# Kernel tuning notes

Measured on AMD Instinct MI355X. Metric: run time of the kernel, lower is better.

The kernel has to match this reference:

```python
import jax, jax.numpy as jnp
import numpy as np

WPB = [4, 2, 2]          # words_per_block per scale
NH = 8                   # num_heads
DIM = 256                # feature dim (uniform, required by cross-scale einsums)
HD = DIM // NH           # per-head feature dim
W_PAR, W_PEER, W_KID = 0.5, 1.0, 2.0


def _linear(x, W):
    # torch nn.Linear (no bias): W is [out, in]
    return jnp.einsum('bhwi,oi->bhwo', x, W)


def _split_heads(y):
    # 'b h w (k f) -> b k h w f'
    b, H, Wd, D = y.shape
    return jnp.transpose(y.reshape(b, H, Wd, NH, D // NH), (0, 3, 1, 2, 4))


def _query(x, W):
    return _split_heads(_linear(x, W))


def _kv(x, W):
    # 'b h w (i k f) -> i b k h w f' with i=2
    y = _linear(x, W)
    b, H, Wd, D = y.shape
    y = y.reshape(b, H, Wd, 2, NH, D // (2 * NH))
    y = jnp.transpose(y, (3, 0, 4, 1, 2, 5))
    return y[0], y[1]


def _blocks(x, hb):
    # 'b k (h1 h2) (w1 w2) f -> b k h1 w1 (h2 w2) f'
    b, k, H, Wd, f = x.shape
    h1, w1 = H // hb, Wd // hb
    x = x.reshape(b, k, h1, hb, w1, hb, f)
    return jnp.transpose(x, (0, 1, 2, 4, 3, 5, 6)).reshape(b, k, h1, w1, hb * hb, f)


def _forward(xs, qpeer, kvpeer, qpar, kvpar, qkid, kvkid):
    n = len(WPB)
    outs = []
    for i in range(n):
        hb = WPB[i]
        hk = WPB[i + 1] if i < n - 1 else 0
        npar = 1 if i > 0 else 0
        scale = (hb + npar + hk) ** -0.5  # coupled scaling (decouple_scales=False)
        x = xs[i]
        b, Hi, Wi, _ = x.shape
        h1, w1 = Hi // hb, Wi // hb
        L = hb * hb  # queries per block
        attn, val, wts = [], [], []
        # --- peers ---
        qp = _blocks(_query(x, qpeer[i]), hb)
        kp, vp = _kv(x, kvpeer[i])
        kp, vp = _blocks(kp, hb), _blocks(vp, hb)
        attn.append(jnp.einsum('bkhwlf,bkhwmf->bkhwlm', qp, kp) * scale)
        val.append(jnp.broadcast_to(vp[:, :, :, :, None], (b, NH, h1, w1, L, L, HD)))
        wts.append(W_PEER * jnp.ones((L,), jnp.float32))
        # --- parents ---
        if i > 0:
            qpa = _blocks(_query(x, qpar[i - 1]), hb)
            kpa, vpa = _kv(xs[i - 1], kvpar[i - 1])  # [b,k,h1,w1,f]
            attn.append(jnp.einsum('bkhwlf,bkhwf->bkhwl', qpa, kpa)[..., None] * scale)
            val.append(jnp.broadcast_to(vpa[:, :, :, :, None, None, :], (b, NH, h1, w1, L, 1, HD)))
            wts.append(W_PAR * jnp.ones((1,), jnp.float32))
        # --- kids ---
        if i < n - 1:
            g = hk * hk
            qk = _query(x, qkid[i])               # [b,k,Hi,Wi,f]
            kk, vk = _kv(xs[i + 1], kvkid[i])
            kkb = _blocks(kk, hk)                  # [b,k,Hi,Wi,g,f]
            a = jnp.einsum('bkhwf,bkhwgf->bkhwg', qk, kkb) * scale
            a = jnp.transpose(a.reshape(b, NH, h1, hb, w1, hb, g), (0, 1, 2, 4, 3, 5, 6)).reshape(b, NH, h1, w1, L, g)
            attn.append(a)
            vkb = vk.reshape(b, NH, h1, hb, hk, w1, hb, hk, HD)
            vkb = jnp.transpose(vkb, (0, 1, 2, 5, 3, 6, 4, 7, 8)).reshape(b, NH, h1, w1, L, g, HD)
            val.append(vkb)
            wts.append(W_KID * jnp.ones((g,), jnp.float32))
        V = jnp.concatenate(val, axis=-2)          # [b,k,h1,w1,L,M,f]
        wvec = jnp.concatenate(wts)                # [M]
        A = jax.nn.softmax(jnp.concatenate(attn, axis=-1), axis=-1)
        A = wvec * A
        A = A / A.sum(-1, keepdims=True)
        # NOTE: faithful to the source einsum 'bkhwlm,bkhwlnf->bkhwlf' where m and n
        # are independently summed indices (attn row-sum times value sum over n).
        o = jnp.einsum('bkhwlm,bkhwlnf->bkhwlf', A, V)
        # 'b k h1 w1 (h2 w2) f -> b (h1 h2) (w1 w2) (k f)'
        o = jnp.transpose(o.reshape(b, NH, h1, w1, hb, hb, HD), (0, 2, 4, 3, 5, 1, 6)).reshape(b, Hi, Wi, NH * HD)
        outs.append(o)
    # forward returns ms_proj_drop(ms_slf_attn): projection output is discarded in the
    # source (ms_out is overwritten), and dropout is identity at p=0.
    return tuple(outs)


def setup_inputs() -> dict:
    key = jax.random.key(0)
    ks = iter(jax.random.split(key, 24))
    B = 8
    Hs = [16, 32, 64]
    d = {}
    for i in range(3):
        d[f'x{i}'] = jax.random.normal(next(ks), (B, Hs[i], Hs[i], DIM), jnp.float32)
    for i in range(3):
        d[f'qpeer_w{i}'] = 0.02 * jax.random.normal(next(ks), (DIM, DIM), jnp.float32)
        d[f'kvpeer_w{i}'] = 0.02 * jax.random.normal(next(ks), (2 * DIM, DIM), jnp.float32)
    for i in (1, 2):
        d[f'qpar_w{i}'] = 0.02 * jax.random.normal(next(ks), (DIM, DIM), jnp.float32)
        d[f'kvpar_w{i}'] = 0.02 * jax.random.normal(next(ks), (2 * DIM, DIM), jnp.float32)
    for i in (0, 1):
        d[f'qkid_w{i}'] = 0.02 * jax.random.normal(next(ks), (DIM, DIM), jnp.float32)
        d[f'kvkid_w{i}'] = 0.02 * jax.random.normal(next(ks), (2 * DIM, DIM), jnp.float32)
    return d


def reference(x0, x1, x2, qpeer_w0, qpeer_w1, qpeer_w2, kvpeer_w0, kvpeer_w1, kvpeer_w2,
              qpar_w1, qpar_w2, kvpar_w1, kvpar_w2, qkid_w0, qkid_w1, kvkid_w0, kvkid_w1):
    return _forward([x0, x1, x2],
                    [qpeer_w0, qpeer_w1, qpeer_w2],
                    [kvpeer_w0, kvpeer_w1, kvpeer_w2],
                    [qpar_w1, qpar_w2],
                    [kvpar_w1, kvpar_w2],
                    [qkid_w0, qkid_w1],
                    [kvkid_w0, kvkid_w1])
```

## Files before the change

### kernel.cpp

```cpp
#include <hip/hip_runtime.h>


constexpr int FD = 256;

typedef __attribute__((ext_vector_type(8))) short short8;
typedef __attribute__((ext_vector_type(4))) float floatx4;

__device__ inline unsigned short bf16bits(float f) {
  unsigned u = __builtin_bit_cast(unsigned, f);
  return (unsigned short)((u + 0x7fffu + ((u >> 16) & 1u)) >> 16);
}
__device__ inline ushort4 cvt4(float4 v) {
  ushort4 o;
  o.x = bf16bits(v.x); o.y = bf16bits(v.y);
  o.z = bf16bits(v.z); o.w = bf16bits(v.w);
  return o;
}

constexpr size_t OFF_S1 = 144 * 256;
constexpr size_t OFF_S2 = OFF_S1 + 2048 * 256;
constexpr size_t OFF_W = OFF_S2 + 8192 * 256;
constexpr size_t OFF_X0 = OFF_W + 7 * 65536;
constexpr size_t OFF_X1 = OFF_X0 + 2048 * 256;

__global__ __launch_bounds__(256) void prep(
    const float4* __restrict__ x0, const float4* __restrict__ x1,
    const float4* __restrict__ x2, const float* __restrict__ wp0,
    const float* __restrict__ wk0, const float* __restrict__ wp1,
    const float* __restrict__ wq1, const float* __restrict__ wk1,
    const float* __restrict__ wp2, const float* __restrict__ wq2,
    unsigned short* __restrict__ ws) {
  int blk = blockIdx.x;
  int t = threadIdx.x;
  if (blk < 2592) {
    const float4* x;
    unsigned short* S;
    unsigned short* xo = nullptr;
    int Hs, Ws, hb, row0;
    if (blk < 32) {
      x = x0; S = ws; xo = ws + OFF_X0; Hs = 4; Ws = 4; hb = 4; row0 = blk * 4;
    } else if (blk < 544) {
      x = x1; S = ws + OFF_S1; xo = ws + OFF_X1;
      Hs = 16; Ws = 16; hb = 2; row0 = (blk - 32) * 4;
    } else {
      x = x2; S = ws + OFF_S2; Hs = 32; Ws = 32; hb = 2; row0 = (blk - 544) * 4;
    }
    int c = t & 63;
    int row = row0 + (t >> 6);
    int bw = row % Ws;
    int t2 = row / Ws;
    int bh = t2 % Hs;
    int b = t2 / Hs;
    int W = Ws * hb;
    size_t base4 = (((size_t)b * Hs * hb + bh * hb) * W + bw * hb) * 64 + c;
    const float4* xb = x + base4;
    float4 s = {0.f, 0.f, 0.f, 0.f};
    for (int i = 0; i < hb; ++i)
      for (int j = 0; j < hb; ++j) {
        float4 v = xb[(size_t)(i * W + j) * 64];
        s.x += v.x; s.y += v.y; s.z += v.z; s.w += v.w;
        if (xo) *(ushort4*)(xo + (base4 + (size_t)(i * W + j) * 64) * 4) = cvt4(v);
      }
    *(ushort4*)(S + (size_t)row * FD + c * 4) = cvt4(s);
  } else {
    int wb = blk - 2592;
    int mat = wb >> 6;
    int row = (wb & 63) * 4 + (t >> 6);
    int c4 = (t & 63) * 4;
    const float* src;
    switch (mat) {
      case 0: src = wp0; break;
      case 1: src = wk0; break;
      case 2: src = wp1; break;
      case 3: src = wq1; break;
      case 4: src = wk1; break;
      case 5: src = wp2; break;
      default: src = wq2; break;
    }
    float4 v = *(const float4*)(src + (size_t)(256 + row) * FD + c4);
    *(ushort4*)(ws + OFF_W + (size_t)mat * 65536 + (size_t)row * FD + c4) =
        cvt4(v);
  }
}

#define MFMA(a, b, c) __builtin_amdgcn_mfma_f32_16x16x32_bf16(a, b, c, 0, 0, 0)

__global__ __launch_bounds__(256) void gemm(const unsigned short* __restrict__ ws,
                                            float* __restrict__ out0,
                                            float* __restrict__ out1,
                                            float* __restrict__ out2) {
  __shared__ float lds[4][16][17];
  int t = threadIdx.x;
  int l = t & 63;
  int wv = t >> 6;
  int c = l & 15, q = l >> 4;
  const short8* Wb = (const short8*)(ws + OFF_W);

  if (blockIdx.x < 512) {
    int r0 = (blockIdx.x >> 2) * 64;
    int n0 = (blockIdx.x & 3) * 64;
    int n = n0 + wv * 16 + c;
    const short8* S2b = (const short8*)(ws + OFF_S2);
    const short8* X1b = (const short8*)(ws + OFF_X1);
    int cb0 = (r0 >> 10) * 256 + (((r0 >> 5) & 31) >> 1) * 16;
    const short8* aS1 = (const short8*)(ws + OFF_S1) + (size_t)(cb0 + c) * 32 + q;
    const short8* aX0 = (const short8*)(ws + OFF_X0) + (size_t)(cb0 + c) * 32 + q;
    const short8 *aS2[4], *aX1[4];
#pragma unroll
    for (int mt = 0; mt < 4; ++mt) {
      aS2[mt] = S2b + (size_t)(r0 + mt * 16 + c) * 32 + q;
      aX1[mt] = X1b + (size_t)(r0 + mt * 16 + c) * 32 + q;
    }
    const short8* bK1 = Wb + (size_t)4 * 8192 + (size_t)n * 32 + q;
    const short8* bP2 = Wb + (size_t)5 * 8192 + (size_t)n * 32 + q;
    const short8* bQ2 = Wb + (size_t)6 * 8192 + (size_t)n * 32 + q;
    const short8* bP1 = Wb + (size_t)2 * 8192 + (size_t)n * 32 + q;
    const short8* bQ1 = Wb + (size_t)3 * 8192 + (size_t)n * 32 + q;
    floatx4 accK[4] = {0, 0, 0, 0};
    floatx4 accC2[4] = {0, 0, 0, 0};
    floatx4 accC1 = {0, 0, 0, 0};
#pragma unroll 2
    for (int kk = 0; kk < 8; ++kk) {
      short8 k1 = bK1[kk * 4], p2 = bP2[kk * 4], q2 = bQ2[kk * 4];
      short8 p1 = bP1[kk * 4], q1 = bQ1[kk * 4];
      accC1 = MFMA(aS1[kk * 4], p1, accC1);
      accC1 = MFMA(aX0[kk * 4], q1, accC1);
#pragma unroll
      for (int mt = 0; mt < 4; ++mt) {
        short8 a = aS2[mt][kk * 4];
        accK[mt] = MFMA(a, k1, accK[mt]);
        accC2[mt] = MFMA(a, p2, accC2[mt]);
        accC2[mt] = MFMA(aX1[mt][kk * 4], q2, accC2[mt]);
      }
    }
#pragma unroll
    for (int r = 0; r < 4; ++r) lds[wv][4 * q + r][c] = accC1[r];
    __syncthreads();
#pragma unroll
    for (int mt = 0; mt < 4; ++mt)
#pragma unroll
      for (int r = 0; r < 4; ++r) {
        int rg = r0 + mt * 16 + 4 * q + r;
        int w = rg & 31;
        out1[(size_t)rg * FD + n] = accK[mt][r] + lds[wv][w >> 1][c];
        int b = rg >> 10, h = (rg >> 5) & 31;
        size_t o = ((size_t)b * 4096 + h * 128 + 2 * w) * FD + n;
        float v = accC2[mt][r];
        out2[o] = v;
        out2[o + FD] = v;
        out2[o + 16384] = v;
        out2[o + 16384 + FD] = v;
      }
  } else {
    int bid = blockIdx.x - 512;
    int r0 = (bid >> 2) * 64;
    int n0 = (bid & 3) * 64;
    int n = n0 + wv * 16 + c;
    const short8* S1b = (const short8*)(ws + OFF_S1);
    const short8* aC = (const short8*)ws + (size_t)((r0 >> 4) + c) * 32 + q;
    const short8* bK = Wb + (size_t)1 * 8192 + (size_t)n * 32 + q;
    const short8* bP = Wb + (size_t)0 * 8192 + (size_t)n * 32 + q;
    const short8* aS[4];
#pragma unroll
    for (int mt = 0; mt < 4; ++mt)
      aS[mt] = S1b + (size_t)(r0 + mt * 16 + c) * 32 + q;
    floatx4 accK[4] = {0, 0, 0, 0};
    floatx4 accC = {0, 0, 0, 0};
#pragma unroll 2
    for (int kk = 0; kk < 8; ++kk) {
      short8 b0 = bK[kk * 4], b1 = bP[kk * 4];
      accC = MFMA(aC[kk * 4], b1, accC);
#pragma unroll
      for (int mt = 0; mt < 4; ++mt) accK[mt] = MFMA(aS[mt][kk * 4], b0, accK[mt]);
    }
    float s0 = __shfl(accC[0], c), s1 = __shfl(accC[1], c);
    float s2 = __shfl(accC[2], c), s3 = __shfl(accC[3], c);
    float cv = q == 0 ? s0 : q == 1 ? s1 : q == 2 ? s2 : s3;
#pragma unroll
    for (int mt = 0; mt < 4; ++mt)
#pragma unroll
      for (int r = 0; r < 4; ++r)
        out0[(size_t)(r0 + mt * 16 + 4 * q + r) * FD + n] = accK[mt][r] + cv;
  }
}

extern "C" void kernel_launch(void* const* d_in, const int* in_sizes, int n_in,
                              void* d_out, int out_size, void* d_ws,
                              size_t ws_size, hipStream_t stream) {
  const float* x0 = (const float*)d_in[0];
  const float* x1 = (const float*)d_in[1];
  const float* x2 = (const float*)d_in[2];

  const float *kvpeer0, *kvpeer1, *kvpeer2, *kvpar1, *kvpar2, *kvkid0, *kvkid1;
  if (n_in > 4 && in_sizes[4] == 2 * FD * FD) {
    kvpeer0 = (const float*)d_in[4];
    kvpeer1 = (const float*)d_in[6];
    kvpeer2 = (const float*)d_in[8];
    kvpar1 = (const float*)d_in[10];
    kvpar2 = (const float*)d_in[12];
    kvkid0 = (const float*)d_in[14];
    kvkid1 = (const float*)d_in[16];
  } else {
    kvpeer0 = (const float*)d_in[6];
    kvpeer1 = (const float*)d_in[7];
    kvpeer2 = (const float*)d_in[8];
    kvpar1 = (const float*)d_in[11];
    kvpar2 = (const float*)d_in[12];
    kvkid0 = (const float*)d_in[15];
    kvkid1 = (const float*)d_in[16];
  }

  unsigned short* ws = (unsigned short*)d_ws;
  float* out0 = (float*)d_out;
  float* out1 = out0 + (size_t)8 * 16 * 16 * FD;
  float* out2 = out1 + (size_t)8 * 32 * 32 * FD;

  prep<<<3040, 256, 0, stream>>>((const float4*)x0, (const float4*)x1,
                                 (const float4*)x2, kvpeer0, kvkid0, kvpeer1,
                                 kvpar1, kvkid1, kvpeer2, kvpar2, ws);
  gemm<<<640, 256, 0, stream>>>(ws, out0, out1, out2);
}
```

Before: 167.7 us.

## Split scale-2 GEMM into separate out1/out2 blocks with register-preloaded operands

```diff
diff --git a/kernel.cpp b/kernel.cpp
--- a/kernel.cpp
+++ b/kernel.cpp
@@ -85,10 +85,9 @@
 
 #define MFMA(a, b, c) __builtin_amdgcn_mfma_f32_16x16x32_bf16(a, b, c, 0, 0, 0)
 
-__global__ __launch_bounds__(256) void gemm(const unsigned short* __restrict__ ws,
-                                            float* __restrict__ out0,
-                                            float* __restrict__ out1,
-                                            float* __restrict__ out2) {
+__global__ __launch_bounds__(256, 2) void gemm(
+    const unsigned short* __restrict__ ws, float* __restrict__ out0,
+    float* __restrict__ out1, float* __restrict__ out2) {
   __shared__ float lds[4][16][17];
   int t = threadIdx.x;
   int l = t & 63;
@@ -100,87 +99,136 @@
     int r0 = (blockIdx.x >> 2) * 64;
     int n0 = (blockIdx.x & 3) * 64;
     int n = n0 + wv * 16 + c;
+    const short8* bP = Wb + (size_t)5 * 8192 + (size_t)n * 32 + q;
+    const short8* bQ = Wb + (size_t)6 * 8192 + (size_t)n * 32 + q;
+    short8 Bp[8], Bq[8];
+#pragma unroll
+    for (int kk = 0; kk < 8; ++kk) {
+      Bp[kk] = bP[kk * 4];
+      Bq[kk] = bQ[kk * 4];
+    }
     const short8* S2b = (const short8*)(ws + OFF_S2);
     const short8* X1b = (const short8*)(ws + OFF_X1);
-    int cb0 = (r0 >> 10) * 256 + (((r0 >> 5) & 31) >> 1) * 16;
-    const short8* aS1 = (const short8*)(ws + OFF_S1) + (size_t)(cb0 + c) * 32 + q;
-    const short8* aX0 = (const short8*)(ws + OFF_X0) + (size_t)(cb0 + c) * 32 + q;
-    const short8 *aS2[4], *aX1[4];
 #pragma unroll
     for (int mt = 0; mt < 4; ++mt) {
-      aS2[mt] = S2b + (size_t)(r0 + mt * 16 + c) * 32 + q;
-      aX1[mt] = X1b + (size_t)(r0 + mt * 16 + c) * 32 + q;
-    }
-    const short8* bK1 = Wb + (size_t)4 * 8192 + (size_t)n * 32 + q;
-    const short8* bP2 = Wb + (size_t)5 * 8192 + (size_t)n * 32 + q;
-    const short8* bQ2 = Wb + (size_t)6 * 8192 + (size_t)n * 32 + q;
-    const short8* bP1 = Wb + (size_t)2 * 8192 + (size_t)n * 32 + q;
-    const short8* bQ1 = Wb + (size_t)3 * 8192 + (size_t)n * 32 + q;
-    floatx4 accK[4] = {0, 0, 0, 0};
-    floatx4 accC2[4] = {0, 0, 0, 0};
-    floatx4 accC1 = {0, 0, 0, 0};
-#pragma unroll 2
-    for (int kk = 0; kk < 8; ++kk) {
-      short8 k1 = bK1[kk * 4], p2 = bP2[kk * 4], q2 = bQ2[kk * 4];
-      short8 p1 = bP1[kk * 4], q1 = bQ1[kk * 4];
-      accC1 = MFMA(aS1[kk * 4], p1, accC1);
-      accC1 = MFMA(aX0[kk * 4], q1, accC1);
-#pragma unroll
-      for (int mt = 0; mt < 4; ++mt) {
-        short8 a = aS2[mt][kk * 4];
-        accK[mt] = MFMA(a, k1, accK[mt]);
-        accC2[mt] = MFMA(a, p2, accC2[mt]);
-        accC2[mt] = MFMA(aX1[mt][kk * 4], q2, accC2[mt]);
-      }
-    }
-#pragma unroll
-    for (int r = 0; r < 4; ++r) lds[wv][4 * q + r][c] = accC1[r];
-    __syncthreads();
-#pragma unroll
-    for (int mt = 0; mt < 4; ++mt)
+      const short8* aS = S2b + (size_t)(r0 + mt * 16 + c) * 32 + q;
+      const short8* aX = X1b + (size_t)(r0 + mt * 16 + c) * 32 + q;
+      short8 As[8], Ax[8];
+#pragma unroll
+      for (int kk = 0; kk < 8; ++kk) {
+        As[kk] = aS[kk * 4];
+        Ax[kk] = aX[kk * 4];
+      }
+      floatx4 acc = {0, 0, 0, 0};
+#pragma unroll
+      for (int kk = 0; kk < 8; ++kk) {
+        acc = MFMA(As[kk], Bp[kk], acc);
+        acc = MFMA(Ax[kk], Bq[kk], acc);
+      }
 #pragma unroll
       for (int r = 0; r < 4; ++r) {
         int rg = r0 + mt * 16 + 4 * q + r;
-        int w = rg & 31;
-        out1[(size_t)rg * FD + n] = accK[mt][r] + lds[wv][w >> 1][c];
-        int b = rg >> 10, h = (rg >> 5) & 31;
+        int b = rg >> 10, h = (rg >> 5) & 31, w = rg & 31;
         size_t o = ((size_t)b * 4096 + h * 128 + 2 * w) * FD + n;
-        float v = accC2[mt][r];
+        float v = acc[r];
         out2[o] = v;
         out2[o + FD] = v;
         out2[o + 16384] = v;
         out2[o + 16384 + FD] = v;
       }
-  } else {
+    }
+  } else if (blockIdx.x < 1024) {
     int bid = blockIdx.x - 512;
     int r0 = (bid >> 2) * 64;
     int n0 = (bid & 3) * 64;
     int n = n0 + wv * 16 + c;
-    const short8* S1b = (const short8*)(ws + OFF_S1);
-    const short8* aC = (const short8*)ws + (size_t)((r0 >> 4) + c) * 32 + q;
+    const short8* bK = Wb + (size_t)4 * 8192 + (size_t)n * 32 + q;
+    const short8* bP = Wb + (size_t)2 * 8192 + (size_t)n * 32 + q;
+    const short8* bQ = Wb + (size_t)3 * 8192 + (size_t)n * 32 + q;
+    short8 Bk[8], Bp[8], Bq[8];
+#pragma unroll
+    for (int kk = 0; kk < 8; ++kk) {
+      Bk[kk] = bK[kk * 4];
+      Bp[kk] = bP[kk * 4];
+      Bq[kk] = bQ[kk * 4];
+    }
+    int cb0 = (r0 >> 10) * 256 + (((r0 >> 5) & 31) >> 1) * 16;
+    {
+      const short8* aS1 =
+          (const short8*)(ws + OFF_S1) + (size_t)(cb0 + c) * 32 + q;
+      const short8* aX0 =
+          (const short8*)(ws + OFF_X0) + (size_t)(cb0 + c) * 32 + q;
+      short8 A1[8], A0[8];
+#pragma unroll
+      for (int kk = 0; kk < 8; ++kk) {
+        A1[kk] = aS1[kk * 4];
+        A0[kk] = aX0[kk * 4];
+      }
+      floatx4 accC = {0, 0, 0, 0};
+#pragma unroll
+      for (int kk = 0; kk < 8; ++kk) {
+        accC = MFMA(A1[kk], Bp[kk], accC);
+        accC = MFMA(A0[kk], Bq[kk], accC);
+      }
+#pragma unroll
+      for (int r = 0; r < 4; ++r) lds[wv][4 * q + r][c] = accC[r];
+    }
+    const short8* S2b = (const short8*)(ws + OFF_S2);
+#pragma unroll
+    for (int mt = 0; mt < 4; ++mt) {
+      const short8* aS = S2b + (size_t)(r0 + mt * 16 + c) * 32 + q;
+      short8 As[8];
+#pragma unroll
+      for (int kk = 0; kk < 8; ++kk) As[kk] = aS[kk * 4];
+      floatx4 acc = {0, 0, 0, 0};
+#pragma unroll
+      for (int kk = 0; kk < 8; ++kk) acc = MFMA(As[kk], Bk[kk], acc);
+#pragma unroll
+      for (int r = 0; r < 4; ++r) {
+        int rg = r0 + mt * 16 + 4 * q + r;
+        int w = rg & 31;
+        out1[(size_t)rg * FD + n] = acc[r] + lds[wv][w >> 1][c];
+      }
+    }
+  } else {
+    int bid = blockIdx.x - 1024;
+    int r0 = (bid >> 2) * 64;
+    int n0 = (bid & 3) * 64;
+    int n = n0 + wv * 16 + c;
     const short8* bK = Wb + (size_t)1 * 8192 + (size_t)n * 32 + q;
     const short8* bP = Wb + (size_t)0 * 8192 + (size_t)n * 32 + q;
-    const short8* aS[4];
-#pragma unroll
-    for (int mt = 0; mt < 4; ++mt)
-      aS[mt] = S1b + (size_t)(r0 + mt * 16 + c) * 32 + q;
-    floatx4 accK[4] = {0, 0, 0, 0};
+    short8 Bk[8], Bp[8];
+#pragma unroll
+    for (int kk = 0; kk < 8; ++kk) {
+      Bk[kk] = bK[kk * 4];
+      Bp[kk] = bP[kk * 4];
+    }
     floatx4 accC = {0, 0, 0, 0};
-#pragma unroll 2
-    for (int kk = 0; kk < 8; ++kk) {
-      short8 b0 = bK[kk * 4], b1 = bP[kk * 4];
-      accC = MFMA(aC[kk * 4], b1, accC);
-#pragma unroll
-      for (int mt = 0; mt < 4; ++mt) accK[mt] = MFMA(aS[mt][kk * 4], b0, accK[mt]);
+    {
+      const short8* aC = (const short8*)ws + (size_t)((r0 >> 4) + c) * 32 + q;
+      short8 AC[8];
+#pragma unroll
+      for (int kk = 0; kk < 8; ++kk) AC[kk] = aC[kk * 4];
+#pragma unroll
+      for (int kk = 0; kk < 8; ++kk) accC = MFMA(AC[kk], Bp[kk], accC);
     }
     float s0 = __shfl(accC[0], c), s1 = __shfl(accC[1], c);
     float s2 = __shfl(accC[2], c), s3 = __shfl(accC[3], c);
     float cv = q == 0 ? s0 : q == 1 ? s1 : q == 2 ? s2 : s3;
-#pragma unroll
-    for (int mt = 0; mt < 4; ++mt)
+    const short8* S1b = (const short8*)(ws + OFF_S1);
+#pragma unroll
+    for (int mt = 0; mt < 4; ++mt) {
+      const short8* aS = S1b + (size_t)(r0 + mt * 16 + c) * 32 + q;
+      short8 As[8];
+#pragma unroll
+      for (int kk = 0; kk < 8; ++kk) As[kk] = aS[kk * 4];
+      floatx4 acc = {0, 0, 0, 0};
+#pragma unroll
+      for (int kk = 0; kk < 8; ++kk) acc = MFMA(As[kk], Bk[kk], acc);
 #pragma unroll
       for (int r = 0; r < 4; ++r)
-        out0[(size_t)(r0 + mt * 16 + 4 * q + r) * FD + n] = accK[mt][r] + cv;
+        out0[(size_t)(r0 + mt * 16 + 4 * q + r) * FD + n] = acc[r] + cv;
+    }
   }
 }
 
@@ -218,5 +266,5 @@
   prep<<<3040, 256, 0, stream>>>((const float4*)x0, (const float4*)x1,
                                  (const float4*)x2, kvpeer0, kvkid0, kvpeer1,
                                  kvpar1, kvkid1, kvpeer2, kvpar2, ws);
-  gemm<<<640, 256, 0, stream>>>(ws, out0, out1, out2);
-}
+  gemm<<<1152, 256, 0, stream>>>(ws, out0, out1, out2);
+}
```

New measurement: 169.8 us. About the same (+1.2%).
